# Performance work log

Measured on AMD Instinct MI355X. Metric: run time of the kernel, lower is better.

Reference implementation:

```python
import jax, jax.numpy as jnp
import numpy as np

B, S, D, H = 1, 4096, 1024, 16
HD = D // H  # 64


def setup_inputs() -> dict:
    key = jax.random.key(0)
    k1, k2, k3, k4, k5 = jax.random.split(key, 5)
    hidden_states = jax.random.normal(k1, (B, S, D), dtype=jnp.float32)
    # rotary frequencies: freqs_cis[s, j] = exp(i * s * theta^(-2j/HD)), stored as (cos, sin)
    inv_freq = 1.0 / (10000.0 ** (jnp.arange(0, HD, 2, dtype=jnp.float32) / HD))  # [HD/2]
    angles = jnp.arange(S, dtype=jnp.float32)[:, None] * inv_freq[None, :]        # [S, HD/2]
    freqs_cis = jnp.stack([jnp.cos(angles), jnp.sin(angles)], axis=-1)            # [S, HD/2, 2]
    attention_mask = jnp.ones((B, S), dtype=jnp.float32)
    scale = 1.0 / np.sqrt(D)
    wq = jax.random.normal(k2, (D, D), dtype=jnp.float32) * scale
    wk = jax.random.normal(k3, (D, D), dtype=jnp.float32) * scale
    wv = jax.random.normal(k4, (D, D), dtype=jnp.float32) * scale
    wo = jax.random.normal(k5, (D, D), dtype=jnp.float32) * scale
    return {"hidden_states": hidden_states, "freqs_cis": freqs_cis,
            "attention_mask": attention_mask, "wq": wq, "wk": wk, "wv": wv, "wo": wo}


def _apply_rope(x, freqs_cis):
    # x: [B, S, H, HD]; freqs_cis: [S, HD/2, 2] (cos, sin)
    b, s, h, hd = x.shape
    xr = x.reshape(b, s, h, hd // 2, 2)
    a, bb = xr[..., 0], xr[..., 1]
    cos = freqs_cis[None, :s, None, :, 0]
    sin = freqs_cis[None, :s, None, :, 1]
    out_r = a * cos - bb * sin
    out_i = a * sin + bb * cos
    return jnp.stack([out_r, out_i], axis=-1).reshape(b, s, h, hd)


def reference(hidden_states, freqs_cis, attention_mask, wq, wk, wv, wo):
    b, s, d = hidden_states.shape
    scaling = HD ** -0.5
    q = (hidden_states @ wq).reshape(b, s, H, HD)
    k = (hidden_states @ wk).reshape(b, s, H, HD)
    v = (hidden_states @ wv).reshape(b, s, H, HD)
    q = _apply_rope(q, freqs_cis)
    k = _apply_rope(k, freqs_cis)
    # [B, H, S, S] scores, exactly as the torch module materializes them
    scores = jnp.einsum('bqhd,bkhd->bhqk', q, k) * scaling
    mask_add = (1.0 - attention_mask)[:, None, None, :] * -10000.0  # [B,1,1,S]
    scores = scores + mask_add
    attn = jax.nn.softmax(scores.astype(jnp.float32), axis=-1).astype(q.dtype)
    out = jnp.einsum('bhqk,bkhd->bqhd', attn, v).reshape(b, s, d)
    return out @ wo
```

## Files before the change

### kernel.cpp

```cpp
#include <hip/hip_runtime.h>
#include <stdint.h>

#define S_LEN 4096
#define DMODEL 1024
#define NH 16
#define HDIM 64
#define KSPLIT 2
#define KCHUNK (S_LEN / KSPLIT)
#define LOG2E 1.44269504088896340736f

typedef __attribute__((ext_vector_type(8))) __bf16 bf16x8;
typedef __attribute__((ext_vector_type(4))) __bf16 bf16x4;
typedef __attribute__((ext_vector_type(2))) __bf16 bf16x2;
typedef __attribute__((ext_vector_type(2))) float f32x2;
typedef __attribute__((ext_vector_type(4))) float f32x4;
typedef __attribute__((ext_vector_type(16))) float f32x16;
typedef __attribute__((ext_vector_type(4))) unsigned int uint32x4;

__device__ __forceinline__ void gload_lds16(const __bf16* g, __bf16* l) {
  __builtin_amdgcn_global_load_lds(
      (const __attribute__((address_space(1))) void*)g,
      (__attribute__((address_space(3))) void*)l, 16, 0, 0);
}

__global__ __launch_bounds__(256) void convert_f32_bf16(const float* __restrict__ src,
                                                        __bf16* __restrict__ dst,
                                                        const float* __restrict__ mask,
                                                        float* __restrict__ maskadd) {
  int idx = blockIdx.x * 256 + threadIdx.x;
  f32x4 v = ((const f32x4*)src)[idx];
  bf16x4 o;
#pragma unroll
  for (int i = 0; i < 4; ++i) o[i] = (__bf16)v[i];
  ((bf16x4*)dst)[idx] = o;
  if (idx < S_LEN) maskadd[idx] = (1.0f - mask[idx]) * (-10000.0f * LOG2E);
}

template <typename T>
__global__ __launch_bounds__(256) void transpose_tiles(const T* __restrict__ src,
                                                       __bf16* __restrict__ dst,
                                                       int R, int C) {
  src += (size_t)blockIdx.z * R * C;
  dst += (size_t)blockIdx.z * R * C;
  __shared__ __bf16 tile[64][65];
  const int r0 = blockIdx.y * 64, c0 = blockIdx.x * 64;
  const int t = threadIdx.x;
  const int col = t & 63, rsub = t >> 6;
#pragma unroll
  for (int i = 0; i < 16; ++i) {
    int r = rsub + i * 4;
    tile[r][col] = (__bf16)src[(size_t)(r0 + r) * C + (c0 + col)];
  }
  __syncthreads();
#pragma unroll
  for (int i = 0; i < 16; ++i) {
    int r = rsub + i * 4;
    dst[(size_t)(c0 + r) * R + (r0 + col)] = tile[col][r];
  }
}

template <int EPI>
__global__ __launch_bounds__(256) void gemm_bt(const __bf16* __restrict__ A,
                                               const __bf16* __restrict__ BT,
                                               __bf16* __restrict__ Cq,
                                               __bf16* __restrict__ Ck,
                                               __bf16* __restrict__ Cvt,
                                               const float* __restrict__ freqs,
                                               float* __restrict__ Cout,
                                               int Kdim, int Ndim) {
  __shared__ __align__(16) __bf16 At[128][32];
  __shared__ __align__(16) __bf16 Bt[128][32];
  const int t = threadIdx.x;
  const int wave = t >> 6, lane = t & 63;
  const int wr = wave >> 1, wc = wave & 1;
  const int lrow = lane & 15, lk = lane >> 4;
  const int bm = blockIdx.x, bn = blockIdx.y;

  f32x4 acc[4][4];
#pragma unroll
  for (int i = 0; i < 4; ++i)
#pragma unroll
    for (int j = 0; j < 4; ++j) acc[i][j] = f32x4{0.f, 0.f, 0.f, 0.f};

  const int arow0 = bm * 128, brow0 = bn * 128;
  const int srow = wave * 16 + (lane >> 2);
  const int scol = (lane & 3) * 8;
  const __bf16* gA0 = &A[(size_t)(arow0 + srow) * Kdim + scol];
  const __bf16* gA1 = &A[(size_t)(arow0 + 64 + srow) * Kdim + scol];
  const __bf16* gB0 = &BT[(size_t)(brow0 + srow) * Kdim + scol];
  const __bf16* gB1 = &BT[(size_t)(brow0 + 64 + srow) * Kdim + scol];
  __bf16* lA0 = &At[wave * 16][0];
  __bf16* lA1 = &At[64 + wave * 16][0];
  __bf16* lB0 = &Bt[wave * 16][0];
  __bf16* lB1 = &Bt[64 + wave * 16][0];

  for (int k0 = 0; k0 < Kdim; k0 += 32) {
    __syncthreads();
    gload_lds16(gA0 + k0, lA0);
    gload_lds16(gA1 + k0, lA1);
    gload_lds16(gB0 + k0, lB0);
    gload_lds16(gB1 + k0, lB1);
    __syncthreads();
    bf16x8 af[4], bfr[4];
#pragma unroll
    for (int mi = 0; mi < 4; ++mi)
      af[mi] = *(const bf16x8*)&At[wr * 64 + mi * 16 + lrow][lk * 8];
#pragma unroll
    for (int ni = 0; ni < 4; ++ni)
      bfr[ni] = *(const bf16x8*)&Bt[wc * 64 + ni * 16 + lrow][lk * 8];
#pragma unroll
    for (int mi = 0; mi < 4; ++mi)
#pragma unroll
      for (int ni = 0; ni < 4; ++ni)
        acc[mi][ni] =
            __builtin_amdgcn_mfma_f32_16x16x32_bf16(af[mi], bfr[ni], acc[mi][ni], 0, 0, 0);
  }

  const int rb = bm * 128 + wr * 64 + lk * 4;
  const int cb = bn * 128 + wc * 64 + lrow;
#pragma unroll
  for (int mi = 0; mi < 4; ++mi)
#pragma unroll
    for (int ni = 0; ni < 4; ++ni) {
      int c = cb + ni * 16;
      if (EPI == 0) {
#pragma unroll
        for (int r = 0; r < 4; ++r)
          Cout[(size_t)(rb + mi * 16 + r) * Ndim + c] = acc[mi][ni][r];
      } else {
        const int type = c >> 10;
        const int d = c & 1023;
        const int hh = d >> 6, hd = d & 63;
        if (type == 2) {
          bf16x4 pk;
#pragma unroll
          for (int r = 0; r < 4; ++r) pk[r] = (__bf16)acc[mi][ni][r];
          *(bf16x4*)&Cvt[((size_t)hh * HDIM + hd) * S_LEN + rb + mi * 16] = pk;
        } else {
          __bf16* dp = (type == 0) ? Cq : Ck;
          const int i = hd >> 1;
          const float sgn = (hd & 1) ? 1.0f : -1.0f;
#pragma unroll
          for (int r = 0; r < 4; ++r) {
            int row = rb + mi * 16 + r;
            float v = acc[mi][ni][r];
            float w = __shfl_xor(v, 1);
            f32x2 cs = *(const f32x2*)&freqs[((size_t)row * 32 + i) * 2];
            float out = fmaf(v, cs[0], sgn * w * cs[1]);
            dp[((size_t)hh * S_LEN + row) * HDIM + hd] = (__bf16)out;
          }
        }
      }
    }
}

template <int KS>
__global__ __launch_bounds__(256, 2) void attn_split(const __bf16* __restrict__ Q,
                                                     const __bf16* __restrict__ Kmat,
                                                     const __bf16* __restrict__ Vt,
                                                     const float* __restrict__ maskadd,
                                                     float* __restrict__ Opart,
                                                     float* __restrict__ Lpart) {
  constexpr int KC = S_LEN / KS;
  __shared__ __align__(16) __bf16 Kl[2][64][64];
  __shared__ __align__(16) __bf16 Vl[2][64][64];

  const int t = threadIdx.x;
  const int id = blockIdx.x;
  const int swz = (id & 7) * (16 * NH * KS / 8) + (id >> 3);
  const int h = swz / (16 * KS);
  const int rem = swz % (16 * KS);
  const int qb = rem / KS;
  const int split = rem % KS;
  const int k0 = split * KC;
  const int wave = t >> 6, lane = t & 63;
  const int lq = lane & 31, hi = lane >> 5;
  const int sw = lq & 7;

  const __bf16* Kh = Kmat + (size_t)h * S_LEN * HDIM;
  const __bf16* Vh = Vt + (size_t)h * HDIM * S_LEN;

  const int sr = t >> 2;
  const int sc0 = (t & 3) * 2;
  const int scs0 = (sc0 ^ (sr & 7)) * 8;
  const int scs1 = ((sc0 + 1) ^ (sr & 7)) * 8;
  const __bf16* Kgb = Kh + (size_t)sr * HDIM + sc0 * 8;
  const __bf16* Vgb = Vh + (size_t)sr * S_LEN + sc0 * 8;

  uint32x4 kreg0, kreg1, vreg0, vreg1;
  kreg0 = *(const uint32x4*)(Kgb + (size_t)k0 * HDIM);
  kreg1 = *(const uint32x4*)(Kgb + (size_t)k0 * HDIM + 8);
  vreg0 = *(const uint32x4*)(Vgb + k0);
  vreg1 = *(const uint32x4*)(Vgb + k0 + 8);
  *(uint32x4*)&Kl[0][sr][scs0] = kreg0;
  *(uint32x4*)&Kl[0][sr][scs1] = kreg1;
  *(uint32x4*)&Vl[0][sr][scs0] = vreg0;
  *(uint32x4*)&Vl[0][sr][scs1] = vreg1;

  const __bf16* Qh = Q + ((size_t)h * S_LEN + qb * 256 + wave * 64 + lq) * HDIM;
  bf16x8 qfA[4], qfB[4];
#pragma unroll
  for (int ds = 0; ds < 4; ++ds) {
    qfA[ds] = *(const bf16x8*)(Qh + ds * 16 + hi * 8);
    qfB[ds] = *(const bf16x8*)(Qh + (size_t)32 * HDIM + ds * 16 + hi * 8);
  }

  __syncthreads();

  const float SCL = 0.125f * LOG2E;
  float lA = 0.f, lB = 0.f;
  f32x16 oA0, oA1, oB0, oB1;
#pragma unroll
  for (int r = 0; r < 16; ++r) { oA0[r] = 0.f; oA1[r] = 0.f; oB0[r] = 0.f; oB1[r] = 0.f; }

  for (int it = 0; it < KC / 64; ++it) {
    const int cur = it & 1;
    const int kb = k0 + it * 64;

    if (it < KC / 64 - 1) {
      kreg0 = *(const uint32x4*)(Kgb + (size_t)(kb + 64) * HDIM);
      kreg1 = *(const uint32x4*)(Kgb + (size_t)(kb + 64) * HDIM + 8);
      vreg0 = *(const uint32x4*)(Vgb + (kb + 64));
      vreg1 = *(const uint32x4*)(Vgb + (kb + 64) + 8);
    }

    f32x16 pA0, pA1, pB0, pB1;
#pragma unroll
    for (int r = 0; r < 16; ++r) { pA0[r] = 0.f; pA1[r] = 0.f; pB0[r] = 0.f; pB1[r] = 0.f; }
    __builtin_amdgcn_s_setprio(1);
#pragma unroll
    for (int ds = 0; ds < 4; ++ds) {
      int sg = ((ds << 1) | hi) ^ sw;
      bf16x8 kf0 = *(const bf16x8*)&Kl[cur][lq][sg * 8];
      pA0 = __builtin_amdgcn_mfma_f32_32x32x16_bf16(kf0, qfA[ds], pA0, 0, 0, 0);
      pB0 = __builtin_amdgcn_mfma_f32_32x32x16_bf16(kf0, qfB[ds], pB0, 0, 0, 0);
    }
#pragma unroll
    for (int ds = 0; ds < 4; ++ds) {
      int sg = ((ds << 1) | hi) ^ sw;
      bf16x8 kf1 = *(const bf16x8*)&Kl[cur][lq + 32][sg * 8];
      pA1 = __builtin_amdgcn_mfma_f32_32x32x16_bf16(kf1, qfA[ds], pA1, 0, 0, 0);
      pB1 = __builtin_amdgcn_mfma_f32_32x32x16_bf16(kf1, qfB[ds], pB1, 0, 0, 0);
    }
    __builtin_amdgcn_s_setprio(0);

#pragma unroll
    for (int tq = 0; tq < 4; ++tq) {
      f32x4 ma0 = *(const f32x4*)&maskadd[kb + tq * 8 + hi * 4];
      f32x4 ma1 = *(const f32x4*)&maskadd[kb + 32 + tq * 8 + hi * 4];
#pragma unroll
      for (int c = 0; c < 4; ++c) {
        pA0[tq * 4 + c] = exp2f(fmaf(pA0[tq * 4 + c], SCL, ma0[c]));
        pB0[tq * 4 + c] = exp2f(fmaf(pB0[tq * 4 + c], SCL, ma0[c]));
        pA1[tq * 4 + c] = exp2f(fmaf(pA1[tq * 4 + c], SCL, ma1[c]));
        pB1[tq * 4 + c] = exp2f(fmaf(pB1[tq * 4 + c], SCL, ma1[c]));
      }
    }
    {
      float a0 = (pA0[0] + pA0[1]) + (pA0[2] + pA0[3]);
      float a1 = (pA0[4] + pA0[5]) + (pA0[6] + pA0[7]);
      float a2 = (pA0[8] + pA0[9]) + (pA0[10] + pA0[11]);
      float a3 = (pA0[12] + pA0[13]) + (pA0[14] + pA0[15]);
      float b0 = (pA1[0] + pA1[1]) + (pA1[2] + pA1[3]);
      float b1 = (pA1[4] + pA1[5]) + (pA1[6] + pA1[7]);
      float b2 = (pA1[8] + pA1[9]) + (pA1[10] + pA1[11]);
      float b3 = (pA1[12] + pA1[13]) + (pA1[14] + pA1[15]);
      float ps = ((a0 + a1) + (a2 + a3)) + ((b0 + b1) + (b2 + b3));
      ps += __shfl_xor(ps, 32);
      lA += ps;
    }
    {
      float a0 = (pB0[0] + pB0[1]) + (pB0[2] + pB0[3]);
      float a1 = (pB0[4] + pB0[5]) + (pB0[6] + pB0[7]);
      float a2 = (pB0[8] + pB0[9]) + (pB0[10] + pB0[11]);
      float a3 = (pB0[12] + pB0[13]) + (pB0[14] + pB0[15]);
      float b0 = (pB1[0] + pB1[1]) + (pB1[2] + pB1[3]);
      float b1 = (pB1[4] + pB1[5]) + (pB1[6] + pB1[7]);
      float b2 = (pB1[8] + pB1[9]) + (pB1[10] + pB1[11]);
      float b3 = (pB1[12] + pB1[13]) + (pB1[14] + pB1[15]);
      float ps = ((a0 + a1) + (a2 + a3)) + ((b0 + b1) + (b2 + b3));
      ps += __shfl_xor(ps, 32);
      lB += ps;
    }

    unsigned int tA0[8], tA1[8], tB0[8], tB1[8];
#pragma unroll
    for (int tp = 0; tp < 8; ++tp) {
      bf16x2 wa0, wa1, wb0, wb1;
      wa0[0] = (__bf16)pA0[2 * tp]; wa0[1] = (__bf16)pA0[2 * tp + 1];
      wa1[0] = (__bf16)pA1[2 * tp]; wa1[1] = (__bf16)pA1[2 * tp + 1];
      wb0[0] = (__bf16)pB0[2 * tp]; wb0[1] = (__bf16)pB0[2 * tp + 1];
      wb1[0] = (__bf16)pB1[2 * tp]; wb1[1] = (__bf16)pB1[2 * tp + 1];
      tA0[tp] = __builtin_bit_cast(unsigned int, wa0);
      tA1[tp] = __builtin_bit_cast(unsigned int, wa1);
      tB0[tp] = __builtin_bit_cast(unsigned int, wb0);
      tB1[tp] = __builtin_bit_cast(unsigned int, wb1);
    }

#pragma unroll
    for (int ks = 0; ks < 4; ++ks) {
      unsigned int a0, a1, a2, a3, b0, b1, b2, b3;
      if (ks == 0)      { a0 = tA0[0]; a1 = tA0[1]; a2 = tA0[2]; a3 = tA0[3];
                          b0 = tB0[0]; b1 = tB0[1]; b2 = tB0[2]; b3 = tB0[3]; }
      else if (ks == 1) { a0 = tA0[4]; a1 = tA0[5]; a2 = tA0[6]; a3 = tA0[7];
                          b0 = tB0[4]; b1 = tB0[5]; b2 = tB0[6]; b3 = tB0[7]; }
      else if (ks == 2) { a0 = tA1[0]; a1 = tA1[1]; a2 = tA1[2]; a3 = tA1[3];
                          b0 = tB1[0]; b1 = tB1[1]; b2 = tB1[2]; b3 = tB1[3]; }
      else              { a0 = tA1[4]; a1 = tA1[5]; a2 = tA1[6]; a3 = tA1[7];
                          b0 = tB1[4]; b1 = tB1[5]; b2 = tB1[6]; b3 = tB1[7]; }
      unsigned int sa0 = hi ? a0 : a2, sa1 = hi ? a1 : a3;
      unsigned int sb0 = hi ? b0 : b2, sb1 = hi ? b1 : b3;
      unsigned int ra0 = (unsigned int)__shfl_xor((int)sa0, 32);
      unsigned int ra1 = (unsigned int)__shfl_xor((int)sa1, 32);
      unsigned int rb0 = (unsigned int)__shfl_xor((int)sb0, 32);
      unsigned int rb1 = (unsigned int)__shfl_xor((int)sb1, 32);
      uint32x4 fa, fb;
      fa[0] = hi ? ra0 : a0; fa[1] = hi ? ra1 : a1;
      fa[2] = hi ? a2 : ra0; fa[3] = hi ? a3 : ra1;
      fb[0] = hi ? rb0 : b0; fb[1] = hi ? rb1 : b1;
      fb[2] = hi ? b2 : rb0; fb[3] = hi ? b3 : rb1;
      bf16x8 fav = __builtin_bit_cast(bf16x8, fa);
      bf16x8 fbv = __builtin_bit_cast(bf16x8, fb);
      int sg = ((ks << 1) | hi) ^ sw;
      bf16x8 v0 = *(const bf16x8*)&Vl[cur][lq][sg * 8];
      bf16x8 v1 = *(const bf16x8*)&Vl[cur][lq + 32][sg * 8];
      __builtin_amdgcn_s_setprio(1);
      oA0 = __builtin_amdgcn_mfma_f32_32x32x16_bf16(v0, fav, oA0, 0, 0, 0);
      oA1 = __builtin_amdgcn_mfma_f32_32x32x16_bf16(v1, fav, oA1, 0, 0, 0);
      oB0 = __builtin_amdgcn_mfma_f32_32x32x16_bf16(v0, fbv, oB0, 0, 0, 0);
      oB1 = __builtin_amdgcn_mfma_f32_32x32x16_bf16(v1, fbv, oB1, 0, 0, 0);
      __builtin_amdgcn_s_setprio(0);
    }

    if (it < KC / 64 - 1) {
      *(uint32x4*)&Kl[cur ^ 1][sr][scs0] = kreg0;
      *(uint32x4*)&Kl[cur ^ 1][sr][scs1] = kreg1;
      *(uint32x4*)&Vl[cur ^ 1][sr][scs0] = vreg0;
      *(uint32x4*)&Vl[cur ^ 1][sr][scs1] = vreg1;
      __syncthreads();
    }
  }

  const int qrowA = qb * 256 + wave * 64 + lq;
  float* OpA = Opart + (((size_t)split * NH + h) * S_LEN + qrowA) * 64;
  float* OpB = OpA + (size_t)32 * 64;
#pragma unroll
  for (int tq = 0; tq < 4; ++tq) {
    f32x4 a, b, c, d;
#pragma unroll
    for (int cc = 0; cc < 4; ++cc) {
      a[cc] = oA0[tq * 4 + cc]; b[cc] = oA1[tq * 4 + cc];
      c[cc] = oB0[tq * 4 + cc]; d[cc] = oB1[tq * 4 + cc];
    }
    *(f32x4*)(OpA + tq * 8 + hi * 4) = a;
    *(f32x4*)(OpA + 32 + tq * 8 + hi * 4) = b;
    *(f32x4*)(OpB + tq * 8 + hi * 4) = c;
    *(f32x4*)(OpB + 32 + tq * 8 + hi * 4) = d;
  }
  if (hi == 0) {
    Lpart[((size_t)split * NH + h) * S_LEN + qrowA] = lA;
    Lpart[((size_t)split * NH + h) * S_LEN + qrowA + 32] = lB;
  }
}

template <int KS>
__global__ __launch_bounds__(256) void attn_merge(const float* __restrict__ Opart,
                                                  const float* __restrict__ Lpart,
                                                  __bf16* __restrict__ AO) {
  int idx = blockIdx.x * 256 + threadIdx.x;
  int dd = (idx & 15) * 4;
  int hq = idx >> 4;
  int q = hq & (S_LEN - 1), h = hq >> 12;
  float l = 0.f;
  f32x4 acc = f32x4{0.f, 0.f, 0.f, 0.f};
#pragma unroll
  for (int s = 0; s < KS; ++s) {
    l += Lpart[(size_t)s * NH * S_LEN + hq];
    f32x4 a = *(const f32x4*)&Opart[((size_t)s * NH * S_LEN + hq) * 64 + dd];
#pragma unroll
    for (int c = 0; c < 4; ++c) acc[c] += a[c];
  }
  float inv = 1.0f / fmaxf(l, 1e-30f);
  bf16x4 o;
#pragma unroll
  for (int c = 0; c < 4; ++c) o[c] = (__bf16)(acc[c] * inv);
  *(bf16x4*)&AO[(size_t)q * DMODEL + h * HDIM + dd] = o;
}

extern "C" void kernel_launch(void* const* d_in, const int* in_sizes, int n_in,
                              void* d_out, int out_size, void* d_ws, size_t ws_size,
                              hipStream_t stream) {
  const float* X = (const float*)d_in[0];
  const float* freqs = (const float*)d_in[1];
  const float* mask = (const float*)d_in[2];
  const float* wq = (const float*)d_in[3];
  const float* wk = (const float*)d_in[4];
  const float* wv = (const float*)d_in[5];
  const float* wo = (const float*)d_in[6];
  float* out = (float*)d_out;

  __bf16* WTqkv = (__bf16*)d_ws;
  __bf16* WoT = WTqkv + 3072 * 1024;
  __bf16* Xb = WoT + 1024 * 1024;
  __bf16* Qb = Xb + (size_t)S_LEN * DMODEL;
  __bf16* Kb = Qb + (size_t)NH * S_LEN * HDIM;
  __bf16* Vtb = Kb + (size_t)NH * S_LEN * HDIM;
  __bf16* AO = Vtb + (size_t)NH * S_LEN * HDIM;

  float* Opart = (float*)(AO + (size_t)S_LEN * DMODEL);
  float* Lpart = Opart + (size_t)KSPLIT * NH * S_LEN * 64;
  float* maskadd = Lpart + (size_t)KSPLIT * NH * S_LEN;

  convert_f32_bf16<<<dim3(S_LEN * DMODEL / 1024), 256, 0, stream>>>(X, Xb, mask, maskadd);

  transpose_tiles<float><<<dim3(16, 16, 1), 256, 0, stream>>>(wq, WTqkv, 1024, 1024);
  transpose_tiles<float><<<dim3(16, 16, 1), 256, 0, stream>>>(wk, WTqkv + 1024 * 1024, 1024, 1024);
  transpose_tiles<float><<<dim3(16, 16, 1), 256, 0, stream>>>(wv, WTqkv + 2 * 1024 * 1024, 1024, 1024);
  transpose_tiles<float><<<dim3(16, 16, 1), 256, 0, stream>>>(wo, WoT, 1024, 1024);

  gemm_bt<1><<<dim3(32, 24), 256, 0, stream>>>(Xb, WTqkv, Qb, Kb, Vtb, freqs, nullptr, 1024, 3072);

  attn_split<KSPLIT><<<dim3(16 * NH * KSPLIT), 256, 0, stream>>>(Qb, Kb, Vtb, maskadd, Opart, Lpart);
  attn_merge<KSPLIT><<<dim3(NH * S_LEN * 16 / 256), 256, 0, stream>>>(Opart, Lpart, AO);

  gemm_bt<0><<<dim3(32, 8), 256, 0, stream>>>(AO, WoT, nullptr, nullptr, nullptr, nullptr, out, 1024, 1024);
}
```

Measured before the change: 204.9 us.

## Stage K/V tiles with direct global-to-LDS loads and 128-key iterations

Replaces register-staged K/V prefetch in the split attention kernel with `global_load_lds` DMA writes straight into shared memory. The XOR swizzle moves from the store side into the per-lane global source addresses. Each iteration now covers 128 keys as two 64-key sub-steps over a larger double buffer, which halves the number of barriers and removes the register round trip for prefetched data. In exchange, LDS use doubles to 64KB per block, which may limit occupancy. Correctness also relies on the barrier properly waiting for the async LDS loads to finish.

```diff
diff --git a/kernel.cpp b/kernel.cpp
--- a/kernel.cpp
+++ b/kernel.cpp
@@ -6,7 +6,6 @@
 #define NH 16
 #define HDIM 64
 #define KSPLIT 2
-#define KCHUNK (S_LEN / KSPLIT)
 #define LOG2E 1.44269504088896340736f
 
 typedef __attribute__((ext_vector_type(8))) __bf16 bf16x8;
@@ -162,8 +161,9 @@
                                                      float* __restrict__ Opart,
                                                      float* __restrict__ Lpart) {
   constexpr int KC = S_LEN / KS;
-  __shared__ __align__(16) __bf16 Kl[2][64][64];
-  __shared__ __align__(16) __bf16 Vl[2][64][64];
+  constexpr int NIT = KC / 128;
+  __shared__ __align__(16) __bf16 Kl[2][128][64];
+  __shared__ __align__(16) __bf16 Vl[2][64][128];
 
   const int t = threadIdx.x;
   const int id = blockIdx.x;
@@ -176,26 +176,29 @@
   const int wave = t >> 6, lane = t & 63;
   const int lq = lane & 31, hi = lane >> 5;
   const int sw = lq & 7;
+  const int swv = lq & 15;
 
   const __bf16* Kh = Kmat + (size_t)h * S_LEN * HDIM;
   const __bf16* Vh = Vt + (size_t)h * HDIM * S_LEN;
 
-  const int sr = t >> 2;
-  const int sc0 = (t & 3) * 2;
-  const int scs0 = (sc0 ^ (sr & 7)) * 8;
-  const int scs1 = ((sc0 + 1) ^ (sr & 7)) * 8;
-  const __bf16* Kgb = Kh + (size_t)sr * HDIM + sc0 * 8;
-  const __bf16* Vgb = Vh + (size_t)sr * S_LEN + sc0 * 8;
-
-  uint32x4 kreg0, kreg1, vreg0, vreg1;
-  kreg0 = *(const uint32x4*)(Kgb + (size_t)k0 * HDIM);
-  kreg1 = *(const uint32x4*)(Kgb + (size_t)k0 * HDIM + 8);
-  vreg0 = *(const uint32x4*)(Vgb + k0);
-  vreg1 = *(const uint32x4*)(Vgb + k0 + 8);
-  *(uint32x4*)&Kl[0][sr][scs0] = kreg0;
-  *(uint32x4*)&Kl[0][sr][scs1] = kreg1;
-  *(uint32x4*)&Vl[0][sr][scs0] = vreg0;
-  *(uint32x4*)&Vl[0][sr][scs1] = vreg1;
+  const int krl = lane >> 3;
+  const __bf16* Kg = Kh + (size_t)(wave * 32 + krl) * HDIM + (((lane & 7) ^ krl) * 8);
+  const int vrl = lane >> 4;
+
+  auto stage = [&](int buf, int kb) {
+#pragma unroll
+    for (int j = 0; j < 4; ++j)
+      gload_lds16(Kg + (size_t)(kb + j * 8) * HDIM, &Kl[buf][wave * 32 + j * 8][0]);
+#pragma unroll
+    for (int i = 0; i < 4; ++i) {
+      const int d15 = i * 4 + vrl;
+      const __bf16* src =
+          Vh + (size_t)(wave * 16 + d15) * S_LEN + kb + (((lane & 15) ^ d15) * 8);
+      gload_lds16(src, &Vl[buf][wave * 16 + i * 4][0]);
+    }
+  };
+
+  stage(0, k0);
 
   const __bf16* Qh = Q + ((size_t)h * S_LEN + qb * 256 + wave * 64 + lq) * HDIM;
   bf16x8 qfA[4], qfB[4];
@@ -213,132 +216,127 @@
 #pragma unroll
   for (int r = 0; r < 16; ++r) { oA0[r] = 0.f; oA1[r] = 0.f; oB0[r] = 0.f; oB1[r] = 0.f; }
 
-  for (int it = 0; it < KC / 64; ++it) {
+  for (int it = 0; it < NIT; ++it) {
     const int cur = it & 1;
-    const int kb = k0 + it * 64;
-
-    if (it < KC / 64 - 1) {
-      kreg0 = *(const uint32x4*)(Kgb + (size_t)(kb + 64) * HDIM);
-      kreg1 = *(const uint32x4*)(Kgb + (size_t)(kb + 64) * HDIM + 8);
-      vreg0 = *(const uint32x4*)(Vgb + (kb + 64));
-      vreg1 = *(const uint32x4*)(Vgb + (kb + 64) + 8);
+    const int kb = k0 + it * 128;
+
+    if (it < NIT - 1) stage(cur ^ 1, kb + 128);
+
+#pragma unroll
+    for (int ksub = 0; ksub < 2; ++ksub) {
+      const int rbase = ksub * 64;
+      const int kbl = kb + ksub * 64;
+
+      f32x16 pA0, pA1, pB0, pB1;
+#pragma unroll
+      for (int r = 0; r < 16; ++r) { pA0[r] = 0.f; pA1[r] = 0.f; pB0[r] = 0.f; pB1[r] = 0.f; }
+      __builtin_amdgcn_s_setprio(1);
+#pragma unroll
+      for (int ds = 0; ds < 4; ++ds) {
+        int sg = ((ds << 1) | hi) ^ sw;
+        bf16x8 kf0 = *(const bf16x8*)&Kl[cur][rbase + lq][sg * 8];
+        pA0 = __builtin_amdgcn_mfma_f32_32x32x16_bf16(kf0, qfA[ds], pA0, 0, 0, 0);
+        pB0 = __builtin_amdgcn_mfma_f32_32x32x16_bf16(kf0, qfB[ds], pB0, 0, 0, 0);
+      }
+#pragma unroll
+      for (int ds = 0; ds < 4; ++ds) {
+        int sg = ((ds << 1) | hi) ^ sw;
+        bf16x8 kf1 = *(const bf16x8*)&Kl[cur][rbase + lq + 32][sg * 8];
+        pA1 = __builtin_amdgcn_mfma_f32_32x32x16_bf16(kf1, qfA[ds], pA1, 0, 0, 0);
+        pB1 = __builtin_amdgcn_mfma_f32_32x32x16_bf16(kf1, qfB[ds], pB1, 0, 0, 0);
+      }
+      __builtin_amdgcn_s_setprio(0);
+
+#pragma unroll
+      for (int tq = 0; tq < 4; ++tq) {
+        f32x4 ma0 = *(const f32x4*)&maskadd[kbl + tq * 8 + hi * 4];
+        f32x4 ma1 = *(const f32x4*)&maskadd[kbl + 32 + tq * 8 + hi * 4];
+#pragma unroll
+        for (int c = 0; c < 4; ++c) {
+          pA0[tq * 4 + c] = exp2f(fmaf(pA0[tq * 4 + c], SCL, ma0[c]));
+          pB0[tq * 4 + c] = exp2f(fmaf(pB0[tq * 4 + c], SCL, ma0[c]));
+          pA1[tq * 4 + c] = exp2f(fmaf(pA1[tq * 4 + c], SCL, ma1[c]));
+          pB1[tq * 4 + c] = exp2f(fmaf(pB1[tq * 4 + c], SCL, ma1[c]));
+        }
+      }
+      {
+        float a0 = (pA0[0] + pA0[1]) + (pA0[2] + pA0[3]);
+        float a1 = (pA0[4] + pA0[5]) + (pA0[6] + pA0[7]);
+        float a2 = (pA0[8] + pA0[9]) + (pA0[10] + pA0[11]);
+        float a3 = (pA0[12] + pA0[13]) + (pA0[14] + pA0[15]);
+        float b0 = (pA1[0] + pA1[1]) + (pA1[2] + pA1[3]);
+        float b1 = (pA1[4] + pA1[5]) + (pA1[6] + pA1[7]);
+        float b2 = (pA1[8] + pA1[9]) + (pA1[10] + pA1[11]);
+        float b3 = (pA1[12] + pA1[13]) + (pA1[14] + pA1[15]);
+        float ps = ((a0 + a1) + (a2 + a3)) + ((b0 + b1) + (b2 + b3));
+        ps += __shfl_xor(ps, 32);
+        lA += ps;
+      }
+      {
+        float a0 = (pB0[0] + pB0[1]) + (pB0[2] + pB0[3]);
+        float a1 = (pB0[4] + pB0[5]) + (pB0[6] + pB0[7]);
+        float a2 = (pB0[8] + pB0[9]) + (pB0[10] + pB0[11]);
+        float a3 = (pB0[12] + pB0[13]) + (pB0[14] + pB0[15]);
+        float b0 = (pB1[0] + pB1[1]) + (pB1[2] + pB1[3]);
+        float b1 = (pB1[4] + pB1[5]) + (pB1[6] + pB1[7]);
+        float b2 = (pB1[8] + pB1[9]) + (pB1[10] + pB1[11]);
+        float b3 = (pB1[12] + pB1[13]) + (pB1[14] + pB1[15]);
+        float ps = ((a0 + a1) + (a2 + a3)) + ((b0 + b1) + (b2 + b3));
+        ps += __shfl_xor(ps, 32);
+        lB += ps;
+      }
+
+      unsigned int tA0[8], tA1[8], tB0[8], tB1[8];
+#pragma unroll
+      for (int tp = 0; tp < 8; ++tp) {
+        bf16x2 wa0, wa1, wb0, wb1;
+        wa0[0] = (__bf16)pA0[2 * tp]; wa0[1] = (__bf16)pA0[2 * tp + 1];
+        wa1[0] = (__bf16)pA1[2 * tp]; wa1[1] = (__bf16)pA1[2 * tp + 1];
+        wb0[0] = (__bf16)pB0[2 * tp]; wb0[1] = (__bf16)pB0[2 * tp + 1];
+        wb1[0] = (__bf16)pB1[2 * tp]; wb1[1] = (__bf16)pB1[2 * tp + 1];
+        tA0[tp] = __builtin_bit_cast(unsigned int, wa0);
+        tA1[tp] = __builtin_bit_cast(unsigned int, wa1);
+        tB0[tp] = __builtin_bit_cast(unsigned int, wb0);
+        tB1[tp] = __builtin_bit_cast(unsigned int, wb1);
+      }
+
+#pragma unroll
+      for (int ks = 0; ks < 4; ++ks) {
+        unsigned int a0, a1, a2, a3, b0, b1, b2, b3;
+        if (ks == 0)      { a0 = tA0[0]; a1 = tA0[1]; a2 = tA0[2]; a3 = tA0[3];
+                            b0 = tB0[0]; b1 = tB0[1]; b2 = tB0[2]; b3 = tB0[3]; }
+        else if (ks == 1) { a0 = tA0[4]; a1 = tA0[5]; a2 = tA0[6]; a3 = tA0[7];
+                            b0 = tB0[4]; b1 = tB0[5]; b2 = tB0[6]; b3 = tB0[7]; }
+        else if (ks == 2) { a0 = tA1[0]; a1 = tA1[1]; a2 = tA1[2]; a3 = tA1[3];
+                            b0 = tB1[0]; b1 = tB1[1]; b2 = tB1[2]; b3 = tB1[3]; }
+        else              { a0 = tA1[4]; a1 = tA1[5]; a2 = tA1[6]; a3 = tA1[7];
+                            b0 = tB1[4]; b1 = tB1[5]; b2 = tB1[6]; b3 = tB1[7]; }
+        unsigned int sa0 = hi ? a0 : a2, sa1 = hi ? a1 : a3;
+        unsigned int sb0 = hi ? b0 : b2, sb1 = hi ? b1 : b3;
+        unsigned int ra0 = (unsigned int)__shfl_xor((int)sa0, 32);
+        unsigned int ra1 = (unsigned int)__shfl_xor((int)sa1, 32);
+        unsigned int rb0 = (unsigned int)__shfl_xor((int)sb0, 32);
+        unsigned int rb1 = (unsigned int)__shfl_xor((int)sb1, 32);
+        uint32x4 fa, fb;
+        fa[0] = hi ? ra0 : a0; fa[1] = hi ? ra1 : a1;
+        fa[2] = hi ? a2 : ra0; fa[3] = hi ? a3 : ra1;
+        fb[0] = hi ? rb0 : b0; fb[1] = hi ? rb1 : b1;
+        fb[2] = hi ? b2 : rb0; fb[3] = hi ? b3 : rb1;
+        bf16x8 fav = __builtin_bit_cast(bf16x8, fa);
+        bf16x8 fbv = __builtin_bit_cast(bf16x8, fb);
+        const int vsg = (ksub * 8 + (ks << 1) + hi) ^ swv;
+        bf16x8 v0 = *(const bf16x8*)&Vl[cur][lq][vsg * 8];
+        bf16x8 v1 = *(const bf16x8*)&Vl[cur][lq + 32][vsg * 8];
+        __builtin_amdgcn_s_setprio(1);
+        oA0 = __builtin_amdgcn_mfma_f32_32x32x16_bf16(v0, fav, oA0, 0, 0, 0);
+        oA1 = __builtin_amdgcn_mfma_f32_32x32x16_bf16(v1, fav, oA1, 0, 0, 0);
+        oB0 = __builtin_amdgcn_mfma_f32_32x32x16_bf16(v0, fbv, oB0, 0, 0, 0);
+        oB1 = __builtin_amdgcn_mfma_f32_32x32x16_bf16(v1, fbv, oB1, 0, 0, 0);
+        __builtin_amdgcn_s_setprio(0);
+      }
     }
 
-    f32x16 pA0, pA1, pB0, pB1;
-#pragma unroll
-    for (int r = 0; r < 16; ++r) { pA0[r] = 0.f; pA1[r] = 0.f; pB0[r] = 0.f; pB1[r] = 0.f; }
-    __builtin_amdgcn_s_setprio(1);
-#pragma unroll
-    for (int ds = 0; ds < 4; ++ds) {
-      int sg = ((ds << 1) | hi) ^ sw;
-      bf16x8 kf0 = *(const bf16x8*)&Kl[cur][lq][sg * 8];
-      pA0 = __builtin_amdgcn_mfma_f32_32x32x16_bf16(kf0, qfA[ds], pA0, 0, 0, 0);
-      pB0 = __builtin_amdgcn_mfma_f32_32x32x16_bf16(kf0, qfB[ds], pB0, 0, 0, 0);
-    }
-#pragma unroll
-    for (int ds = 0; ds < 4; ++ds) {
-      int sg = ((ds << 1) | hi) ^ sw;
-      bf16x8 kf1 = *(const bf16x8*)&Kl[cur][lq + 32][sg * 8];
-      pA1 = __builtin_amdgcn_mfma_f32_32x32x16_bf16(kf1, qfA[ds], pA1, 0, 0, 0);
-      pB1 = __builtin_amdgcn_mfma_f32_32x32x16_bf16(kf1, qfB[ds], pB1, 0, 0, 0);
-    }
-    __builtin_amdgcn_s_setprio(0);
-
-#pragma unroll
-    for (int tq = 0; tq < 4; ++tq) {
-      f32x4 ma0 = *(const f32x4*)&maskadd[kb + tq * 8 + hi * 4];
-      f32x4 ma1 = *(const f32x4*)&maskadd[kb + 32 + tq * 8 + hi * 4];
-#pragma unroll
-      for (int c = 0; c < 4; ++c) {
-        pA0[tq * 4 + c] = exp2f(fmaf(pA0[tq * 4 + c], SCL, ma0[c]));
-        pB0[tq * 4 + c] = exp2f(fmaf(pB0[tq * 4 + c], SCL, ma0[c]));
-        pA1[tq * 4 + c] = exp2f(fmaf(pA1[tq * 4 + c], SCL, ma1[c]));
-        pB1[tq * 4 + c] = exp2f(fmaf(pB1[tq * 4 + c], SCL, ma1[c]));
-      }
-    }
-    {
-      float a0 = (pA0[0] + pA0[1]) + (pA0[2] + pA0[3]);
-      float a1 = (pA0[4] + pA0[5]) + (pA0[6] + pA0[7]);
-      float a2 = (pA0[8] + pA0[9]) + (pA0[10] + pA0[11]);
-      float a3 = (pA0[12] + pA0[13]) + (pA0[14] + pA0[15]);
-      float b0 = (pA1[0] + pA1[1]) + (pA1[2] + pA1[3]);
-      float b1 = (pA1[4] + pA1[5]) + (pA1[6] + pA1[7]);
-      float b2 = (pA1[8] + pA1[9]) + (pA1[10] + pA1[11]);
-      float b3 = (pA1[12] + pA1[13]) + (pA1[14] + pA1[15]);
-      float ps = ((a0 + a1) + (a2 + a3)) + ((b0 + b1) + (b2 + b3));
-      ps += __shfl_xor(ps, 32);
-      lA += ps;
-    }
-    {
-      float a0 = (pB0[0] + pB0[1]) + (pB0[2] + pB0[3]);
-      float a1 = (pB0[4] + pB0[5]) + (pB0[6] + pB0[7]);
-      float a2 = (pB0[8] + pB0[9]) + (pB0[10] + pB0[11]);
-      float a3 = (pB0[12] + pB0[13]) + (pB0[14] + pB0[15]);
-      float b0 = (pB1[0] + pB1[1]) + (pB1[2] + pB1[3]);
-      float b1 = (pB1[4] + pB1[5]) + (pB1[6] + pB1[7]);
-      float b2 = (pB1[8] + pB1[9]) + (pB1[10] + pB1[11]);
-      float b3 = (pB1[12] + pB1[13]) + (pB1[14] + pB1[15]);
-      float ps = ((a0 + a1) + (a2 + a3)) + ((b0 + b1) + (b2 + b3));
-      ps += __shfl_xor(ps, 32);
-      lB += ps;
-    }
-
-    unsigned int tA0[8], tA1[8], tB0[8], tB1[8];
-#pragma unroll
-    for (int tp = 0; tp < 8; ++tp) {
-      bf16x2 wa0, wa1, wb0, wb1;
-      wa0[0] = (__bf16)pA0[2 * tp]; wa0[1] = (__bf16)pA0[2 * tp + 1];
-      wa1[0] = (__bf16)pA1[2 * tp]; wa1[1] = (__bf16)pA1[2 * tp + 1];
-      wb0[0] = (__bf16)pB0[2 * tp]; wb0[1] = (__bf16)pB0[2 * tp + 1];
-      wb1[0] = (__bf16)pB1[2 * tp]; wb1[1] = (__bf16)pB1[2 * tp + 1];
-      tA0[tp] = __builtin_bit_cast(unsigned int, wa0);
-      tA1[tp] = __builtin_bit_cast(unsigned int, wa1);
-      tB0[tp] = __builtin_bit_cast(unsigned int, wb0);
-      tB1[tp] = __builtin_bit_cast(unsigned int, wb1);
-    }
-
-#pragma unroll
-    for (int ks = 0; ks < 4; ++ks) {
-      unsigned int a0, a1, a2, a3, b0, b1, b2, b3;
-      if (ks == 0)      { a0 = tA0[0]; a1 = tA0[1]; a2 = tA0[2]; a3 = tA0[3];
-                          b0 = tB0[0]; b1 = tB0[1]; b2 = tB0[2]; b3 = tB0[3]; }
-      else if (ks == 1) { a0 = tA0[4]; a1 = tA0[5]; a2 = tA0[6]; a3 = tA0[7];
-                          b0 = tB0[4]; b1 = tB0[5]; b2 = tB0[6]; b3 = tB0[7]; }
-      else if (ks == 2) { a0 = tA1[0]; a1 = tA1[1]; a2 = tA1[2]; a3 = tA1[3];
-                          b0 = tB1[0]; b1 = tB1[1]; b2 = tB1[2]; b3 = tB1[3]; }
-      else              { a0 = tA1[4]; a1 = tA1[5]; a2 = tA1[6]; a3 = tA1[7];
-                          b0 = tB1[4]; b1 = tB1[5]; b2 = tB1[6]; b3 = tB1[7]; }
-      unsigned int sa0 = hi ? a0 : a2, sa1 = hi ? a1 : a3;
-      unsigned int sb0 = hi ? b0 : b2, sb1 = hi ? b1 : b3;
-      unsigned int ra0 = (unsigned int)__shfl_xor((int)sa0, 32);
-      unsigned int ra1 = (unsigned int)__shfl_xor((int)sa1, 32);
-      unsigned int rb0 = (unsigned int)__shfl_xor((int)sb0, 32);
-      unsigned int rb1 = (unsigned int)__shfl_xor((int)sb1, 32);
-      uint32x4 fa, fb;
-      fa[0] = hi ? ra0 : a0; fa[1] = hi ? ra1 : a1;
-      fa[2] = hi ? a2 : ra0; fa[3] = hi ? a3 : ra1;
-      fb[0] = hi ? rb0 : b0; fb[1] = hi ? rb1 : b1;
-      fb[2] = hi ? b2 : rb0; fb[3] = hi ? b3 : rb1;
-      bf16x8 fav = __builtin_bit_cast(bf16x8, fa);
-      bf16x8 fbv = __builtin_bit_cast(bf16x8, fb);
-      int sg = ((ks << 1) | hi) ^ sw;
-      bf16x8 v0 = *(const bf16x8*)&Vl[cur][lq][sg * 8];
-      bf16x8 v1 = *(const bf16x8*)&Vl[cur][lq + 32][sg * 8];
-      __builtin_amdgcn_s_setprio(1);
-      oA0 = __builtin_amdgcn_mfma_f32_32x32x16_bf16(v0, fav, oA0, 0, 0, 0);
-      oA1 = __builtin_amdgcn_mfma_f32_32x32x16_bf16(v1, fav, oA1, 0, 0, 0);
-      oB0 = __builtin_amdgcn_mfma_f32_32x32x16_bf16(v0, fbv, oB0, 0, 0, 0);
-      oB1 = __builtin_amdgcn_mfma_f32_32x32x16_bf16(v1, fbv, oB1, 0, 0, 0);
-      __builtin_amdgcn_s_setprio(0);
-    }
-
-    if (it < KC / 64 - 1) {
-      *(uint32x4*)&Kl[cur ^ 1][sr][scs0] = kreg0;
-      *(uint32x4*)&Kl[cur ^ 1][sr][scs1] = kreg1;
-      *(uint32x4*)&Vl[cur ^ 1][sr][scs0] = vreg0;
-      *(uint32x4*)&Vl[cur ^ 1][sr][scs1] = vreg1;
-      __syncthreads();
-    }
+    if (it < NIT - 1) __syncthreads();
   }
 
   const int qrowA = qb * 256 + wave * 64 + lq;
```

New measurement: 228.6 us. 1.12x slower.
